# Optimization experiments

Hardware: AMD Instinct MI355X
Metric: run time of the kernel (lower is better)

## Reference

```python
import jax, jax.numpy as jnp
import numpy as np

B, D_IN, D, H, HD, M = 4096, 512, 128, 8, 16, 128
L = M + 1            # 1 query token + M memory slots
D_FF = 512
SCALE = 0.25         # 1/sqrt(HD)


def _ln(x, w, b, eps=1e-5):
    m = jnp.mean(x, axis=-1, keepdims=True)
    v = jnp.var(x, axis=-1, keepdims=True)
    return (x - m) * jax.lax.rsqrt(v + eps) * w + b


def setup_inputs() -> dict:
    ks = jax.random.split(jax.random.key(0), 26)
    n = lambda i, shape, s=1.0: jax.random.normal(ks[i], shape, jnp.float32) * s
    return {
        "x": n(0, (B, 1, D_IN)),
        "W_in": n(1, (D, D_IN), 0.05),
        "b_in": n(2, (D,), 0.02),
        "pos": n(3, (B, 1, D), 0.02),
        "mask": jnp.zeros((B, M), jnp.float32),  # additive attention bias for memory slots
        "mem": n(5, (B, M, D)),
        "ln1_w": jnp.ones((D,), jnp.float32), "ln1_b": jnp.zeros((D,), jnp.float32),
        "W_qkv": n(8, (3 * D, D), 0.09),
        "b_qkv": n(9, (3 * D,), 0.02),
        "W_out": n(10, (D, D), 0.09),
        "b_out": n(11, (D,), 0.02),
        "ln2_w": jnp.ones((D,), jnp.float32), "ln2_b": jnp.zeros((D,), jnp.float32),
        "ln3_w": jnp.ones((D,), jnp.float32), "ln3_b": jnp.zeros((D,), jnp.float32),
        "W_ff1": n(16, (D_FF, D), 0.09),
        "b_ff1": n(17, (D_FF,), 0.02),
        "ln4_w": jnp.ones((D_FF,), jnp.float32), "ln4_b": jnp.zeros((D_FF,), jnp.float32),
        "W_ff2": n(20, (D, D_FF), 0.04),
        "b_ff2": n(21, (D,), 0.02),
        "ln5_w": jnp.ones((D,), jnp.float32), "ln5_b": jnp.zeros((D,), jnp.float32),
        "W_head": n(24, (D_IN, D), 0.09),
        "b_head": n(25, (D_IN,), 0.02),
    }


def reference(x, W_in, b_in, pos, mask, mem, ln1_w, ln1_b, W_qkv, b_qkv,
              W_out, b_out, ln2_w, ln2_b, ln3_w, ln3_b, W_ff1, b_ff1,
              ln4_w, ln4_b, W_ff2, b_ff2, ln5_w, ln5_b, W_head, b_head):
    Bn = x.shape[0]
    # input projection + positional offset -> single query token per row  [B,1,D]
    q_in = (x.reshape(Bn, D_IN) @ W_in.T + b_in)[:, None, :] + pos
    # additive attention bias: 0 for the query slot, `mask` for memory slots  [B,L]
    bias = jnp.concatenate([jnp.zeros((Bn, 1), x.dtype), mask], axis=1)
    kv_in = jnp.concatenate([q_in, mem], axis=1)           # [B,L,D]
    kv_ln = _ln(kv_in, ln1_w, ln1_b)
    Wq, Wkv = W_qkv[:D], W_qkv[D:]
    bq, bkv = b_qkv[:D], b_qkv[D:]
    q = q_in[:, 0] @ Wq.T + bq                             # [B,D]  (Q uses UN-normalized q_in)
    kv = kv_ln @ Wkv.T + bkv                               # [B,L,2D]
    k, v = kv[..., :D], kv[..., D:]
    qh = q.reshape(Bn, H, HD)
    kh = k.reshape(Bn, L, H, HD)
    vh = v.reshape(Bn, L, H, HD)
    scores = jnp.einsum('bhd,blhd->bhl', qh * SCALE, kh) + bias[:, None, :]
    p = jax.nn.softmax(scores, axis=-1)                    # [B,H,L]
    o = jnp.einsum('bhl,blhd->bhd', p, vh).reshape(Bn, D)
    attn = _ln((o @ W_out.T + b_out)[:, None, :], ln2_w, ln2_b)
    h = attn + q_in                                        # residual  [B,1,D]
    f = _ln(h, ln3_w, ln3_b) @ W_ff1.T + b_ff1             # [B,1,D_FF]
    f = 0.5 * f * (1.0 + jax.lax.erf(f * 0.7071067811865476))  # exact GELU
    f = _ln(f, ln4_w, ln4_b) @ W_ff2.T + b_ff2             # [B,1,D]
    h2 = _ln(f + h, ln5_w, ln5_b)
    return h2 @ W_head.T + b_head                          # [B,1,D_IN]
```

## Files before the change

kernel.cpp:

```cpp
#include <hip/hip_runtime.h>

namespace {

constexpr int Dn   = 128;
constexpr int DIN  = 512;
constexpr int Hn   = 8;
constexpr int Mn   = 128;
constexpr int DFF  = 512;
constexpr int Gn   = 4;
constexpr float ATT_SCALE = 0.25f;
constexpr float INV_SQRT2 = 0.70710678118654752440f;

__device__ __forceinline__ float dot128(const float* __restrict__ wrow,
                                        const float* __restrict__ v)
{
    const float4* w4 = (const float4*)wrow;
    const float4* v4 = (const float4*)v;
    float acc = 0.f;
#pragma unroll
    for (int j = 0; j < 32; ++j) {
        float4 a = w4[j], b = v4[j];
        acc += a.x*b.x + a.y*b.y + a.z*b.z + a.w*b.w;
    }
    return acc;
}

template <int NCOL, int TPR>
__device__ __forceinline__ void ln_row(const float* __restrict__ src,
                                       float* __restrict__ dst,
                                       const float* __restrict__ gw,
                                       const float* __restrict__ gb,
                                       const float* __restrict__ resid,
                                       int sub)
{
    constexpr int E = NCOL / TPR;
    float v0[E]; float sm = 0.f;
#pragma unroll
    for (int i = 0; i < E; ++i) { v0[i] = src[sub*E + i]; sm += v0[i]; }
#pragma unroll
    for (int m = TPR/2; m >= 1; m >>= 1) sm += __shfl_xor(sm, m, TPR);
    float mean = sm * (1.f / (float)NCOL);
    float vs = 0.f;
#pragma unroll
    for (int i = 0; i < E; ++i) { float d0 = v0[i] - mean; vs += d0*d0; }
#pragma unroll
    for (int m = TPR/2; m >= 1; m >>= 1) vs += __shfl_xor(vs, m, TPR);
    float rstd = rsqrtf(vs * (1.f / (float)NCOL) + 1e-5f);
#pragma unroll
    for (int i = 0; i < E; ++i) {
        int d = sub*E + i;
        float r = (v0[i] - mean) * rstd * gw[d] + gb[d];
        dst[d] = resid ? (r + resid[d]) : r;
    }
}

__global__ __launch_bounds__(256, 2)
void fused_block(const float* __restrict__ x,
                 const float* __restrict__ W_in,
                 const float* __restrict__ b_in,
                 const float* __restrict__ pos,
                 const float* __restrict__ mask,
                 const float* __restrict__ mem,
                 const float* __restrict__ ln1_w, const float* __restrict__ ln1_b,
                 const float* __restrict__ W_qkv, const float* __restrict__ b_qkv,
                 const float* __restrict__ W_out, const float* __restrict__ b_out,
                 const float* __restrict__ ln2_w, const float* __restrict__ ln2_b,
                 const float* __restrict__ ln3_w, const float* __restrict__ ln3_b,
                 const float* __restrict__ W_ff1, const float* __restrict__ b_ff1,
                 const float* __restrict__ ln4_w, const float* __restrict__ ln4_b,
                 const float* __restrict__ W_ff2, const float* __restrict__ b_ff2,
                 const float* __restrict__ ln5_w, const float* __restrict__ ln5_b,
                 const float* __restrict__ W_head, const float* __restrict__ b_head,
                 float* __restrict__ out)
{
    const int t    = threadIdx.x;
    const int b0   = blockIdx.x * Gn;
    const int lane = t & 63;
    const int wv   = t >> 6;

    __shared__ __align__(16) float s_mem[Mn * Dn];
    __shared__ __align__(16) float s_A [Hn][Dn];
    __shared__ __align__(16) float s_sc[Hn][Mn];
    __shared__ __align__(16) float s_rstd[Mn];
    __shared__ __align__(16) float s_lnq[Dn];
    __shared__ __align__(16) float s_q  [Dn];
    __shared__ __align__(16) float s_qin[Gn][Dn];
    __shared__ __align__(16) float s_hh [Gn][Dn];
    __shared__ __align__(16) float s_qo [Gn][Dn];
    __shared__ float s_s1[Hn], s_s2c[Hn], s_s0[Hn], s_den[Hn], s_p0[Hn];

    float4* mem4 = (float4*)s_mem;
    float (*s_tmp)[Dn] = (float(*)[Dn])&s_sc[0][0];

    {
        const float4* src = (const float4*)(x + (size_t)b0 * DIN);
        mem4[t]       = src[t];
        mem4[t + 256] = src[t + 256];
    }
    __syncthreads();

    if (t < Dn) {
        const float4* w4 = (const float4*)(W_in + (size_t)t * DIN);
        float acc[Gn] = {0.f, 0.f, 0.f, 0.f};
        for (int j = 0; j < DIN/4; ++j) {
            float4 a = w4[j];
#pragma unroll
            for (int g = 0; g < Gn; ++g) {
                float4 xv = mem4[g*(DIN/4) + j];
                acc[g] = fmaf(a.x, xv.x, acc[g]); acc[g] = fmaf(a.y, xv.y, acc[g]);
                acc[g] = fmaf(a.z, xv.z, acc[g]); acc[g] = fmaf(a.w, xv.w, acc[g]);
            }
        }
#pragma unroll
        for (int g = 0; g < Gn; ++g)
            s_qin[g][t] = acc[g] + b_in[t] + pos[(size_t)(b0+g)*Dn + t];
    }
    __syncthreads();

    for (int g = 0; g < Gn; ++g) {
        __syncthreads();

        {
            const float4* src = (const float4*)(mem + (size_t)(b0+g) * Mn * Dn);
#pragma unroll
            for (int i = 0; i < 16; ++i) {
                int fid = t + 256*i;
                int r = fid >> 5, k = fid & 31;
                mem4[r*32 + (k ^ (r & 7))] = src[fid];
            }
        }
        if (t < 64) {
            ln_row<Dn, 64>(&s_qin[g][0], s_lnq, ln1_w, ln1_b, nullptr, t);
        } else if (t >= 128) {
            int dd = t - 128;
            s_q[dd] = dot128(W_qkv + (size_t)dd*Dn, &s_qin[g][0]) + b_qkv[dd];
        }
        __syncthreads();

        {
            int h = t >> 5, js = t & 31;
            float aq[4] = {0.f, 0.f, 0.f, 0.f};
            float ch = 0.f;
#pragma unroll
            for (int d0 = 0; d0 < 16; ++d0) {
                float qv = s_q[h*16 + d0];
                float4 w = ((const float4*)(W_qkv + (size_t)(Dn + h*16 + d0)*Dn))[js];
                aq[0] = fmaf(qv, w.x, aq[0]); aq[1] = fmaf(qv, w.y, aq[1]);
                aq[2] = fmaf(qv, w.z, aq[2]); aq[3] = fmaf(qv, w.w, aq[3]);
                ch = fmaf(qv, b_qkv[Dn + h*16 + d0], ch);
            }
            float s1p = 0.f, s2p = 0.f, s0p = 0.f;
            float aqw[4];
#pragma unroll
            for (int c = 0; c < 4; ++c) {
                int j = 4*js + c;
                float a = ATT_SCALE * aq[c];
                aqw[c] = a * ln1_w[j];
                s1p += aqw[c];
                s2p = fmaf(a, ln1_b[j], s2p);
                s0p = fmaf(a, s_lnq[j], s0p);
            }
            *(float4*)&s_A[h][4*js] = make_float4(aqw[0], aqw[1], aqw[2], aqw[3]);
            ch *= ATT_SCALE;
#pragma unroll
            for (int m = 16; m >= 1; m >>= 1) {
                s1p += __shfl_xor(s1p, m, 32);
                s2p += __shfl_xor(s2p, m, 32);
                s0p += __shfl_xor(s0p, m, 32);
            }
            if (js == 0) { s_s1[h] = s1p; s_s2c[h] = s2p + ch; s_s0[h] = s0p + ch; }
        }
        __syncthreads();
        {
            int h = t >> 5;
            float sub = s_s1[h] * (1.f/128.f);
            float4* p = (float4*)&s_A[0][0] + t;
            float4 v = *p;
            v.x -= sub; v.y -= sub; v.z -= sub; v.w -= sub;
            *p = v;
        }
        __syncthreads();

        {
            int r = t >> 1, hf = t & 1;
            float d[Hn];
#pragma unroll
            for (int h = 0; h < Hn; ++h) d[h] = 0.f;
            float sum = 0.f, ssq = 0.f;
#pragma unroll
            for (int kk = 0; kk < 16; ++kk) {
                int k = hf*16 + kk;
                float4 v = mem4[r*32 + (k ^ (r & 7))];
                sum += v.x + v.y + v.z + v.w;
                ssq = fmaf(v.x, v.x, ssq); ssq = fmaf(v.y, v.y, ssq);
                ssq = fmaf(v.z, v.z, ssq); ssq = fmaf(v.w, v.w, ssq);
#pragma unroll
                for (int h = 0; h < Hn; ++h) {
                    float4 a = ((const float4*)&s_A[h][0])[k];
                    d[h] = fmaf(a.x, v.x, d[h]); d[h] = fmaf(a.y, v.y, d[h]);
                    d[h] = fmaf(a.z, v.z, d[h]); d[h] = fmaf(a.w, v.w, d[h]);
                }
            }
            sum += __shfl_xor(sum, 1);
            ssq += __shfl_xor(ssq, 1);
#pragma unroll
            for (int h = 0; h < Hn; ++h) d[h] += __shfl_xor(d[h], 1);
            if (hf == 0) {
                float mean = sum * (1.f/128.f);
                float var  = fmaf(-mean, mean, ssq * (1.f/128.f));
                float rstd = rsqrtf(var + 1e-5f);
                float msk  = mask[(size_t)(b0+g)*Mn + r];
                s_rstd[r] = rstd;
#pragma unroll
                for (int h = 0; h < Hn; ++h)
                    s_sc[h][r] = fmaf(rstd, d[h], s_s2c[h]) + msk;
            }
        }
        __syncthreads();

        {
            int h = t >> 5, s = t & 31;
            float4 sv = ((float4*)&s_sc[h][0])[s];
            float s0 = s_s0[h];
            float mx = fmaxf(fmaxf(sv.x, sv.y), fmaxf(sv.z, sv.w));
#pragma unroll
            for (int m = 16; m >= 1; m >>= 1) mx = fmaxf(mx, __shfl_xor(mx, m, 32));
            mx = fmaxf(mx, s0);
            float e0 = __expf(sv.x - mx), e1 = __expf(sv.y - mx);
            float e2 = __expf(sv.z - mx), e3 = __expf(sv.w - mx);
            float ds = e0 + e1 + e2 + e3;
#pragma unroll
            for (int m = 16; m >= 1; m >>= 1) ds += __shfl_xor(ds, m, 32);
            float p0 = __expf(s0 - mx);
            float4 rs = ((float4*)s_rstd)[s];
            ((float4*)&s_sc[h][0])[s] =
                make_float4(e0*rs.x, e1*rs.y, e2*rs.z, e3*rs.w);
            if (s == 0) { s_den[h] = ds + p0; s_p0[h] = p0; }
        }
        __syncthreads();

        {
            int w = t >> 6, l = t & 63;
            int h0 = 2*w, h1 = 2*w + 1;
            int slot = l >> 1, half = l & 1;
            float c00 = 0.f, c01 = 0.f, c10 = 0.f, c11 = 0.f;
#pragma unroll 4
            for (int r = 0; r < Mn; ++r) {
                float2 mv = *(const float2*)(s_mem + r*Dn + ((slot ^ (r & 7)) << 2) + half*2);
                float q0 = s_sc[h0][r], q1 = s_sc[h1][r];
                c00 = fmaf(q0, mv.x, c00); c01 = fmaf(q0, mv.y, c01);
                c10 = fmaf(q1, mv.x, c10); c11 = fmaf(q1, mv.y, c11);
            }
            float r0 = c00 + c01, r1 = c10 + c11;
#pragma unroll
            for (int m = 1; m < 64; m <<= 1) {
                r0 += __shfl_xor(r0, m);
                r1 += __shfl_xor(r1, m);
            }
            float cS0 = r0 * (1.f/128.f), cS1 = r1 * (1.f/128.f);
            int j0 = 2*l, j1 = 2*l + 1;
            float den0 = s_den[h0], p00 = s_p0[h0], sP0 = den0 - p00, inv0 = 1.f/den0;
            float den1 = s_den[h1], p01 = s_p0[h1], sP1 = den1 - p01, inv1 = 1.f/den1;
            float lq0 = s_lnq[j0], lq1 = s_lnq[j1];
            float w0 = ln1_w[j0], w1 = ln1_w[j1];
            float bb0 = ln1_b[j0], bb1 = ln1_b[j1];
            *(float2*)&s_A[h0][j0] =
                make_float2((p00*lq0 + w0*(c00 - cS0) + bb0*sP0) * inv0,
                            (p00*lq1 + w1*(c01 - cS0) + bb1*sP0) * inv0);
            *(float2*)&s_A[h1][j0] =
                make_float2((p01*lq0 + w0*(c10 - cS1) + bb0*sP1) * inv1,
                            (p01*lq1 + w1*(c11 - cS1) + bb1*sP1) * inv1);
        }
        __syncthreads();

        if (t < Dn) {
            int h = t >> 4;
            s_qo[g][t] = dot128(W_qkv + (size_t)(2*Dn + t)*Dn, &s_A[h][0])
                       + b_qkv[2*Dn + t];
        }
    }
    __syncthreads();

    if (t < Dn) {
        const float4* w4 = (const float4*)(W_out + (size_t)t * Dn);
        float acc[Gn] = {0.f, 0.f, 0.f, 0.f};
#pragma unroll 8
        for (int j = 0; j < 32; ++j) {
            float4 a = w4[j];
#pragma unroll
            for (int g = 0; g < Gn; ++g) {
                float4 v = ((const float4*)&s_qo[g][0])[j];
                acc[g] = fmaf(a.x, v.x, acc[g]); acc[g] = fmaf(a.y, v.y, acc[g]);
                acc[g] = fmaf(a.z, v.z, acc[g]); acc[g] = fmaf(a.w, v.w, acc[g]);
            }
        }
#pragma unroll
        for (int g = 0; g < Gn; ++g) s_tmp[g][t] = acc[g] + b_out[t];
    }
    __syncthreads();

    ln_row<Dn, 64>(&s_tmp[wv][0], &s_hh[wv][0], ln2_w, ln2_b, &s_qin[wv][0], lane);
    __syncthreads();

    ln_row<Dn, 64>(&s_hh[wv][0], &s_qin[wv][0], ln3_w, ln3_b, nullptr, lane);
    __syncthreads();

    {
        int e0 = t, e1 = t + 256;
        const float4* wa = (const float4*)(W_ff1 + (size_t)e0 * Dn);
        const float4* wb = (const float4*)(W_ff1 + (size_t)e1 * Dn);
        float acc0[Gn] = {0.f,0.f,0.f,0.f}, acc1[Gn] = {0.f,0.f,0.f,0.f};
#pragma unroll 4
        for (int j = 0; j < 32; ++j) {
            float4 a = wa[j], b = wb[j];
#pragma unroll
            for (int g = 0; g < Gn; ++g) {
                float4 v = ((const float4*)&s_qin[g][0])[j];
                acc0[g] = fmaf(a.x, v.x, acc0[g]); acc0[g] = fmaf(a.y, v.y, acc0[g]);
                acc0[g] = fmaf(a.z, v.z, acc0[g]); acc0[g] = fmaf(a.w, v.w, acc0[g]);
                acc1[g] = fmaf(b.x, v.x, acc1[g]); acc1[g] = fmaf(b.y, v.y, acc1[g]);
                acc1[g] = fmaf(b.z, v.z, acc1[g]); acc1[g] = fmaf(b.w, v.w, acc1[g]);
            }
        }
#pragma unroll
        for (int g = 0; g < Gn; ++g) {
            float v0 = acc0[g] + b_ff1[e0];
            float v1 = acc1[g] + b_ff1[e1];
            s_mem[g*DFF + e0] = 0.5f * v0 * (1.f + erff(v0 * INV_SQRT2));
            s_mem[g*DFF + e1] = 0.5f * v1 * (1.f + erff(v1 * INV_SQRT2));
        }
    }
    __syncthreads();

    ln_row<DFF, 64>(s_mem + wv*DFF, s_mem + wv*DFF, ln4_w, ln4_b, nullptr, lane);
    __syncthreads();

    if (t < Dn) {
        const float4* w4 = (const float4*)(W_ff2 + (size_t)t * DFF);
        float acc[Gn] = {0.f, 0.f, 0.f, 0.f};
#pragma unroll 4
        for (int j = 0; j < DFF/4; ++j) {
            float4 a = w4[j];
#pragma unroll
            for (int g = 0; g < Gn; ++g) {
                float4 v = ((const float4*)(s_mem + g*DFF))[j];
                acc[g] = fmaf(a.x, v.x, acc[g]); acc[g] = fmaf(a.y, v.y, acc[g]);
                acc[g] = fmaf(a.z, v.z, acc[g]); acc[g] = fmaf(a.w, v.w, acc[g]);
            }
        }
#pragma unroll
        for (int g = 0; g < Gn; ++g)
            s_tmp[g][t] = acc[g] + b_ff2[t] + s_hh[g][t];
    }
    __syncthreads();

    ln_row<Dn, 64>(&s_tmp[wv][0], &s_qo[wv][0], ln5_w, ln5_b, nullptr, lane);
    __syncthreads();

    {
        int e0 = t, e1 = t + 256;
        const float4* wa = (const float4*)(W_head + (size_t)e0 * Dn);
        const float4* wb = (const float4*)(W_head + (size_t)e1 * Dn);
        float acc0[Gn] = {0.f,0.f,0.f,0.f}, acc1[Gn] = {0.f,0.f,0.f,0.f};
#pragma unroll 4
        for (int j = 0; j < 32; ++j) {
            float4 a = wa[j], b = wb[j];
#pragma unroll
            for (int g = 0; g < Gn; ++g) {
                float4 v = ((const float4*)&s_qo[g][0])[j];
                acc0[g] = fmaf(a.x, v.x, acc0[g]); acc0[g] = fmaf(a.y, v.y, acc0[g]);
                acc0[g] = fmaf(a.z, v.z, acc0[g]); acc0[g] = fmaf(a.w, v.w, acc0[g]);
                acc1[g] = fmaf(b.x, v.x, acc1[g]); acc1[g] = fmaf(b.y, v.y, acc1[g]);
                acc1[g] = fmaf(b.z, v.z, acc1[g]); acc1[g] = fmaf(b.w, v.w, acc1[g]);
            }
        }
#pragma unroll
        for (int g = 0; g < Gn; ++g) {
            out[(size_t)(b0+g)*DIN + e0] = acc0[g] + b_head[e0];
            out[(size_t)(b0+g)*DIN + e1] = acc1[g] + b_head[e1];
        }
    }
}

}

extern "C" void kernel_launch(void* const* d_in, const int* in_sizes, int n_in,
                              void* d_out, int out_size, void* d_ws, size_t ws_size,
                              hipStream_t stream)
{
    const float* x      = (const float*)d_in[0];
    const float* W_in   = (const float*)d_in[1];
    const float* b_in   = (const float*)d_in[2];
    const float* pos    = (const float*)d_in[3];
    const float* mask   = (const float*)d_in[4];
    const float* mem    = (const float*)d_in[5];
    const float* ln1_w  = (const float*)d_in[6];
    const float* ln1_b  = (const float*)d_in[7];
    const float* W_qkv  = (const float*)d_in[8];
    const float* b_qkv  = (const float*)d_in[9];
    const float* W_out  = (const float*)d_in[10];
    const float* b_out  = (const float*)d_in[11];
    const float* ln2_w  = (const float*)d_in[12];
    const float* ln2_b  = (const float*)d_in[13];
    const float* ln3_w  = (const float*)d_in[14];
    const float* ln3_b  = (const float*)d_in[15];
    const float* W_ff1  = (const float*)d_in[16];
    const float* b_ff1  = (const float*)d_in[17];
    const float* ln4_w  = (const float*)d_in[18];
    const float* ln4_b  = (const float*)d_in[19];
    const float* W_ff2  = (const float*)d_in[20];
    const float* b_ff2  = (const float*)d_in[21];
    const float* ln5_w  = (const float*)d_in[22];
    const float* ln5_b  = (const float*)d_in[23];
    const float* W_head = (const float*)d_in[24];
    const float* b_head = (const float*)d_in[25];

    const int B = in_sizes[0] / DIN;
    fused_block<<<dim3(B / Gn), dim3(256), 0, stream>>>(
        x, W_in, b_in, pos, mask, mem,
        ln1_w, ln1_b, W_qkv, b_qkv, W_out, b_out,
        ln2_w, ln2_b, ln3_w, ln3_b,
        W_ff1, b_ff1, ln4_w, ln4_b, W_ff2, b_ff2,
        ln5_w, ln5_b, W_head, b_head,
        (float*)d_out);
}
```

Baseline: 283.7 us.

## Process eight rows per block with 512 threads, split-K GEMVs and bf16 staging

Doubles the batch rows handled per block to eight and the block size to 512 threads, so each weight load is reused across more rows. The input and FF2 projections become split-K reductions through shared memory, the attention score and context stages are regrouped with one head per wave, and the per-head query-weight vector and attention output are stored in shared memory as bf16. This cuts global weight traffic per row and the number of barriers per row. In exchange it adds shared-memory reduction passes, precision loss from the bf16 rounding, and register pressure under the 512-thread launch bound.

```diff
diff --git a/kernel.cpp b/kernel.cpp
--- a/kernel.cpp
+++ b/kernel.cpp
@@ -7,9 +7,18 @@
 constexpr int Hn   = 8;
 constexpr int Mn   = 128;
 constexpr int DFF  = 512;
-constexpr int Gn   = 4;
+constexpr int Gn   = 8;
 constexpr float ATT_SCALE = 0.25f;
 constexpr float INV_SQRT2 = 0.70710678118654752440f;
+
+__device__ __forceinline__ unsigned short f2bf(float f) {
+    unsigned u = __float_as_uint(f);
+    unsigned r = (u + 0x7fffu + ((u >> 16) & 1u)) >> 16;
+    return (unsigned short)r;
+}
+__device__ __forceinline__ float bf2f(unsigned short s) {
+    return __uint_as_float((unsigned)s << 16);
+}
 
 __device__ __forceinline__ float dot128(const float* __restrict__ wrow,
                                         const float* __restrict__ v)
@@ -25,26 +34,26 @@
     return acc;
 }
 
-template <int NCOL, int TPR>
-__device__ __forceinline__ void ln_row(const float* __restrict__ src,
-                                       float* __restrict__ dst,
-                                       const float* __restrict__ gw,
-                                       const float* __restrict__ gb,
-                                       const float* __restrict__ resid,
-                                       int sub)
+template <int NCOL>
+__device__ __forceinline__ void ln_row64(const float* __restrict__ src,
+                                         float* __restrict__ dst,
+                                         const float* __restrict__ gw,
+                                         const float* __restrict__ gb,
+                                         const float* __restrict__ resid,
+                                         int sub)
 {
-    constexpr int E = NCOL / TPR;
+    constexpr int E = NCOL / 64;
     float v0[E]; float sm = 0.f;
 #pragma unroll
     for (int i = 0; i < E; ++i) { v0[i] = src[sub*E + i]; sm += v0[i]; }
 #pragma unroll
-    for (int m = TPR/2; m >= 1; m >>= 1) sm += __shfl_xor(sm, m, TPR);
+    for (int m = 32; m >= 1; m >>= 1) sm += __shfl_xor(sm, m);
     float mean = sm * (1.f / (float)NCOL);
     float vs = 0.f;
 #pragma unroll
     for (int i = 0; i < E; ++i) { float d0 = v0[i] - mean; vs += d0*d0; }
 #pragma unroll
-    for (int m = TPR/2; m >= 1; m >>= 1) vs += __shfl_xor(vs, m, TPR);
+    for (int m = 32; m >= 1; m >>= 1) vs += __shfl_xor(vs, m);
     float rstd = rsqrtf(vs * (1.f / (float)NCOL) + 1e-5f);
 #pragma unroll
     for (int i = 0; i < E; ++i) {
@@ -54,7 +63,7 @@
     }
 }
 
-__global__ __launch_bounds__(256, 2)
+__global__ __launch_bounds__(512, 2)
 void fused_block(const float* __restrict__ x,
                  const float* __restrict__ W_in,
                  const float* __restrict__ b_in,
@@ -79,67 +88,65 @@
     const int wv   = t >> 6;
 
     __shared__ __align__(16) float s_mem[Mn * Dn];
-    __shared__ __align__(16) float s_A [Hn][Dn];
-    __shared__ __align__(16) float s_sc[Hn][Mn];
-    __shared__ __align__(16) float s_rstd[Mn];
-    __shared__ __align__(16) float s_lnq[Dn];
-    __shared__ __align__(16) float s_q  [Dn];
+    __shared__ __align__(16) float s_A[1024];
+    __shared__ __align__(16) float s_sc[1152];
+    __shared__ __align__(16) float s_lnq[128];
     __shared__ __align__(16) float s_qin[Gn][Dn];
-    __shared__ __align__(16) float s_hh [Gn][Dn];
-    __shared__ __align__(16) float s_qo [Gn][Dn];
-    __shared__ float s_s1[Hn], s_s2c[Hn], s_s0[Hn], s_den[Hn], s_p0[Hn];
+    __shared__ __align__(16) unsigned short s_qo16[Gn][Dn];
+    __shared__ float s_s2c[Hn], s_s0[Hn], s_den[Hn], s_p0[Hn];
 
     float4* mem4 = (float4*)s_mem;
-    float (*s_tmp)[Dn] = (float(*)[Dn])&s_sc[0][0];
-
-    {
-        const float4* src = (const float4*)(x + (size_t)b0 * DIN);
-        mem4[t]       = src[t];
-        mem4[t + 256] = src[t + 256];
-    }
-    __syncthreads();
-
-    if (t < Dn) {
-        const float4* w4 = (const float4*)(W_in + (size_t)t * DIN);
-        float acc[Gn] = {0.f, 0.f, 0.f, 0.f};
-        for (int j = 0; j < DIN/4; ++j) {
+    unsigned short* s_At = (unsigned short*)s_A;
+    float* s_q = s_sc;
+
+    {
+        int d = t & 127, kg = t >> 7;
+        const float4* w4 = (const float4*)(W_in + (size_t)d * DIN) + kg*32;
+        float acc[8] = {0,0,0,0,0,0,0,0};
+        for (int j = 0; j < 32; ++j) {
             float4 a = w4[j];
 #pragma unroll
-            for (int g = 0; g < Gn; ++g) {
-                float4 xv = mem4[g*(DIN/4) + j];
+            for (int g = 0; g < 8; ++g) {
+                float4 xv = *(const float4*)(x + (size_t)(b0+g)*DIN + (size_t)(kg*32+j)*4);
                 acc[g] = fmaf(a.x, xv.x, acc[g]); acc[g] = fmaf(a.y, xv.y, acc[g]);
                 acc[g] = fmaf(a.z, xv.z, acc[g]); acc[g] = fmaf(a.w, xv.w, acc[g]);
             }
         }
 #pragma unroll
-        for (int g = 0; g < Gn; ++g)
-            s_qin[g][t] = acc[g] + b_in[t] + pos[(size_t)(b0+g)*Dn + t];
+        for (int g = 0; g < 8; ++g) s_mem[kg*1024 + d*8 + g] = acc[g];
+    }
+    __syncthreads();
+    {
+#pragma unroll
+        for (int u = 0; u < 2; ++u) {
+            int idx = t*2 + u; int d = idx >> 3, g = idx & 7;
+            float v = s_mem[idx] + s_mem[1024 + idx] + s_mem[2048 + idx] + s_mem[3072 + idx];
+            s_qin[g][d] = v + b_in[d] + pos[(size_t)(b0+g)*Dn + d];
+        }
     }
     __syncthreads();
 
     for (int g = 0; g < Gn; ++g) {
-        __syncthreads();
-
         {
             const float4* src = (const float4*)(mem + (size_t)(b0+g) * Mn * Dn);
 #pragma unroll
-            for (int i = 0; i < 16; ++i) {
-                int fid = t + 256*i;
+            for (int i = 0; i < 8; ++i) {
+                int fid = t + 512*i;
                 int r = fid >> 5, k = fid & 31;
                 mem4[r*32 + (k ^ (r & 7))] = src[fid];
             }
-        }
-        if (t < 64) {
-            ln_row<Dn, 64>(&s_qin[g][0], s_lnq, ln1_w, ln1_b, nullptr, t);
-        } else if (t >= 128) {
-            int dd = t - 128;
-            s_q[dd] = dot128(W_qkv + (size_t)dd*Dn, &s_qin[g][0]) + b_qkv[dd];
-        }
-        __syncthreads();
-
-        {
+            if (t < 64) {
+                ln_row64<Dn>(&s_qin[g][0], s_lnq, ln1_w, ln1_b, nullptr, t);
+            } else if (t >= 128 && t < 256) {
+                int dd = t - 128;
+                s_q[dd] = dot128(W_qkv + (size_t)dd*Dn, &s_qin[g][0]) + b_qkv[dd];
+            }
+        }
+        __syncthreads();
+
+        if (t < 256) {
             int h = t >> 5, js = t & 31;
-            float aq[4] = {0.f, 0.f, 0.f, 0.f};
+            float aq[4] = {0,0,0,0};
             float ch = 0.f;
 #pragma unroll
             for (int d0 = 0; d0 < 16; ++d0) {
@@ -149,235 +156,282 @@
                 aq[2] = fmaf(qv, w.z, aq[2]); aq[3] = fmaf(qv, w.w, aq[3]);
                 ch = fmaf(qv, b_qkv[Dn + h*16 + d0], ch);
             }
+            ch *= ATT_SCALE;
             float s1p = 0.f, s2p = 0.f, s0p = 0.f;
             float aqw[4];
 #pragma unroll
             for (int c = 0; c < 4; ++c) {
-                int j = 4*js + c;
+                int j = js*4 + c;
                 float a = ATT_SCALE * aq[c];
                 aqw[c] = a * ln1_w[j];
                 s1p += aqw[c];
                 s2p = fmaf(a, ln1_b[j], s2p);
                 s0p = fmaf(a, s_lnq[j], s0p);
             }
-            *(float4*)&s_A[h][4*js] = make_float4(aqw[0], aqw[1], aqw[2], aqw[3]);
-            ch *= ATT_SCALE;
 #pragma unroll
             for (int m = 16; m >= 1; m >>= 1) {
                 s1p += __shfl_xor(s1p, m, 32);
                 s2p += __shfl_xor(s2p, m, 32);
                 s0p += __shfl_xor(s0p, m, 32);
             }
-            if (js == 0) { s_s1[h] = s1p; s_s2c[h] = s2p + ch; s_s0[h] = s0p + ch; }
-        }
-        __syncthreads();
-        {
-            int h = t >> 5;
-            float sub = s_s1[h] * (1.f/128.f);
-            float4* p = (float4*)&s_A[0][0] + t;
-            float4 v = *p;
-            v.x -= sub; v.y -= sub; v.z -= sub; v.w -= sub;
-            *p = v;
-        }
-        __syncthreads();
-
-        {
-            int r = t >> 1, hf = t & 1;
-            float d[Hn];
-#pragma unroll
-            for (int h = 0; h < Hn; ++h) d[h] = 0.f;
+            float sub = s1p * (1.f/128.f);
+#pragma unroll
+            for (int c = 0; c < 4; ++c) {
+                int j = js*4 + c;
+                s_At[j*8 + h] = f2bf(aqw[c] - sub);
+            }
+            if (js == 0) { s_s2c[h] = s2p + ch; s_s0[h] = s0p + ch; }
+        }
+        __syncthreads();
+
+        {
+            int r = t >> 2, hf = t & 3;
+            float d8[8] = {0,0,0,0,0,0,0,0};
             float sum = 0.f, ssq = 0.f;
 #pragma unroll
-            for (int kk = 0; kk < 16; ++kk) {
-                int k = hf*16 + kk;
+            for (int kk = 0; kk < 8; ++kk) {
+                int k = hf*8 + kk;
                 float4 v = mem4[r*32 + (k ^ (r & 7))];
                 sum += v.x + v.y + v.z + v.w;
                 ssq = fmaf(v.x, v.x, ssq); ssq = fmaf(v.y, v.y, ssq);
                 ssq = fmaf(v.z, v.z, ssq); ssq = fmaf(v.w, v.w, ssq);
 #pragma unroll
-                for (int h = 0; h < Hn; ++h) {
-                    float4 a = ((const float4*)&s_A[h][0])[k];
-                    d[h] = fmaf(a.x, v.x, d[h]); d[h] = fmaf(a.y, v.y, d[h]);
-                    d[h] = fmaf(a.z, v.z, d[h]); d[h] = fmaf(a.w, v.w, d[h]);
+                for (int c = 0; c < 4; ++c) {
+                    int j = k*4 + c;
+                    uint4 au = *(const uint4*)&s_At[j*8];
+                    float a0 = __uint_as_float(au.x << 16);
+                    float a1 = __uint_as_float(au.x & 0xffff0000u);
+                    float a2 = __uint_as_float(au.y << 16);
+                    float a3 = __uint_as_float(au.y & 0xffff0000u);
+                    float a4 = __uint_as_float(au.z << 16);
+                    float a5 = __uint_as_float(au.z & 0xffff0000u);
+                    float a6 = __uint_as_float(au.w << 16);
+                    float a7 = __uint_as_float(au.w & 0xffff0000u);
+                    float vc = (c == 0) ? v.x : (c == 1) ? v.y : (c == 2) ? v.z : v.w;
+                    d8[0] = fmaf(a0, vc, d8[0]); d8[1] = fmaf(a1, vc, d8[1]);
+                    d8[2] = fmaf(a2, vc, d8[2]); d8[3] = fmaf(a3, vc, d8[3]);
+                    d8[4] = fmaf(a4, vc, d8[4]); d8[5] = fmaf(a5, vc, d8[5]);
+                    d8[6] = fmaf(a6, vc, d8[6]); d8[7] = fmaf(a7, vc, d8[7]);
                 }
             }
-            sum += __shfl_xor(sum, 1);
-            ssq += __shfl_xor(ssq, 1);
-#pragma unroll
-            for (int h = 0; h < Hn; ++h) d[h] += __shfl_xor(d[h], 1);
+#pragma unroll
+            for (int m = 1; m <= 2; m <<= 1) {
+                sum += __shfl_xor(sum, m, 4);
+                ssq += __shfl_xor(ssq, m, 4);
+#pragma unroll
+                for (int h = 0; h < 8; ++h) d8[h] += __shfl_xor(d8[h], m, 4);
+            }
             if (hf == 0) {
                 float mean = sum * (1.f/128.f);
                 float var  = fmaf(-mean, mean, ssq * (1.f/128.f));
                 float rstd = rsqrtf(var + 1e-5f);
-                float msk  = mask[(size_t)(b0+g)*Mn + r];
-                s_rstd[r] = rstd;
-#pragma unroll
-                for (int h = 0; h < Hn; ++h)
-                    s_sc[h][r] = fmaf(rstd, d[h], s_s2c[h]) + msk;
-            }
-        }
-        __syncthreads();
-
-        {
-            int h = t >> 5, s = t & 31;
-            float4 sv = ((float4*)&s_sc[h][0])[s];
-            float s0 = s_s0[h];
-            float mx = fmaxf(fmaxf(sv.x, sv.y), fmaxf(sv.z, sv.w));
-#pragma unroll
-            for (int m = 16; m >= 1; m >>= 1) mx = fmaxf(mx, __shfl_xor(mx, m, 32));
-            mx = fmaxf(mx, s0);
-            float e0 = __expf(sv.x - mx), e1 = __expf(sv.y - mx);
-            float e2 = __expf(sv.z - mx), e3 = __expf(sv.w - mx);
-            float ds = e0 + e1 + e2 + e3;
-#pragma unroll
-            for (int m = 16; m >= 1; m >>= 1) ds += __shfl_xor(ds, m, 32);
-            float p0 = __expf(s0 - mx);
-            float4 rs = ((float4*)s_rstd)[s];
-            ((float4*)&s_sc[h][0])[s] =
-                make_float4(e0*rs.x, e1*rs.y, e2*rs.z, e3*rs.w);
-            if (s == 0) { s_den[h] = ds + p0; s_p0[h] = p0; }
-        }
-        __syncthreads();
-
-        {
-            int w = t >> 6, l = t & 63;
-            int h0 = 2*w, h1 = 2*w + 1;
-            int slot = l >> 1, half = l & 1;
-            float c00 = 0.f, c01 = 0.f, c10 = 0.f, c11 = 0.f;
+#pragma unroll
+                for (int h = 0; h < 8; ++h) s_sc[r*9 + h] = d8[h];
+                s_sc[r*9 + 8] = rstd;
+            }
+        }
+        __syncthreads();
+
+        {
+            int w = wv, l = lane;
+            int r0 = 2*l, r1 = 2*l + 1;
+            float raw0 = s_sc[r0*9 + w], rs0 = s_sc[r0*9 + 8];
+            float raw1 = s_sc[r1*9 + w], rs1 = s_sc[r1*9 + 8];
+            float mk0 = mask[(size_t)(b0+g)*Mn + r0];
+            float mk1 = mask[(size_t)(b0+g)*Mn + r1];
+            float sc0 = fmaf(rs0, raw0, s_s2c[w]) + mk0;
+            float sc1 = fmaf(rs1, raw1, s_s2c[w]) + mk1;
+            float mx = fmaxf(sc0, sc1);
+#pragma unroll
+            for (int m = 1; m < 64; m <<= 1) mx = fmaxf(mx, __shfl_xor(mx, m));
+            mx = fmaxf(mx, s_s0[w]);
+            float e0 = __expf(sc0 - mx), e1 = __expf(sc1 - mx);
+            float ds = e0 + e1;
+#pragma unroll
+            for (int m = 1; m < 64; m <<= 1) ds += __shfl_xor(ds, m);
+            float p0 = __expf(s_s0[w] - mx);
+            s_A[r0*8 + w] = e0 * rs0;
+            s_A[r1*8 + w] = e1 * rs1;
+            if (l == 0) { s_den[w] = ds + p0; s_p0[w] = p0; }
+        }
+        __syncthreads();
+
+        float ctx0[8], ctx1[8];
+        {
+            int w = wv, l = lane;
+#pragma unroll
+            for (int h = 0; h < 8; ++h) { ctx0[h] = 0.f; ctx1[h] = 0.f; }
 #pragma unroll 4
-            for (int r = 0; r < Mn; ++r) {
-                float2 mv = *(const float2*)(s_mem + r*Dn + ((slot ^ (r & 7)) << 2) + half*2);
-                float q0 = s_sc[h0][r], q1 = s_sc[h1][r];
-                c00 = fmaf(q0, mv.x, c00); c01 = fmaf(q0, mv.y, c01);
-                c10 = fmaf(q1, mv.x, c10); c11 = fmaf(q1, mv.y, c11);
-            }
-            float r0 = c00 + c01, r1 = c10 + c11;
-#pragma unroll
-            for (int m = 1; m < 64; m <<= 1) {
-                r0 += __shfl_xor(r0, m);
-                r1 += __shfl_xor(r1, m);
-            }
-            float cS0 = r0 * (1.f/128.f), cS1 = r1 * (1.f/128.f);
-            int j0 = 2*l, j1 = 2*l + 1;
-            float den0 = s_den[h0], p00 = s_p0[h0], sP0 = den0 - p00, inv0 = 1.f/den0;
-            float den1 = s_den[h1], p01 = s_p0[h1], sP1 = den1 - p01, inv1 = 1.f/den1;
-            float lq0 = s_lnq[j0], lq1 = s_lnq[j1];
-            float w0 = ln1_w[j0], w1 = ln1_w[j1];
-            float bb0 = ln1_b[j0], bb1 = ln1_b[j1];
-            *(float2*)&s_A[h0][j0] =
-                make_float2((p00*lq0 + w0*(c00 - cS0) + bb0*sP0) * inv0,
-                            (p00*lq1 + w1*(c01 - cS0) + bb1*sP0) * inv0);
-            *(float2*)&s_A[h1][j0] =
-                make_float2((p01*lq0 + w0*(c10 - cS1) + bb0*sP1) * inv1,
-                            (p01*lq1 + w1*(c11 - cS1) + bb1*sP1) * inv1);
-        }
-        __syncthreads();
-
-        if (t < Dn) {
+            for (int rr = 0; rr < 16; ++rr) {
+                int r = w*16 + rr;
+                float4 qa = *(const float4*)&s_A[r*8];
+                float4 qb = *(const float4*)&s_A[r*8 + 4];
+                const float* bp = s_mem + r*Dn + (((l>>1) ^ (r & 7)) << 2) + (l & 1)*2;
+                float2 mv = *(const float2*)bp;
+                ctx0[0]=fmaf(qa.x,mv.x,ctx0[0]); ctx1[0]=fmaf(qa.x,mv.y,ctx1[0]);
+                ctx0[1]=fmaf(qa.y,mv.x,ctx0[1]); ctx1[1]=fmaf(qa.y,mv.y,ctx1[1]);
+                ctx0[2]=fmaf(qa.z,mv.x,ctx0[2]); ctx1[2]=fmaf(qa.z,mv.y,ctx1[2]);
+                ctx0[3]=fmaf(qa.w,mv.x,ctx0[3]); ctx1[3]=fmaf(qa.w,mv.y,ctx1[3]);
+                ctx0[4]=fmaf(qb.x,mv.x,ctx0[4]); ctx1[4]=fmaf(qb.x,mv.y,ctx1[4]);
+                ctx0[5]=fmaf(qb.y,mv.x,ctx0[5]); ctx1[5]=fmaf(qb.y,mv.y,ctx1[5]);
+                ctx0[6]=fmaf(qb.z,mv.x,ctx0[6]); ctx1[6]=fmaf(qb.z,mv.y,ctx1[6]);
+                ctx0[7]=fmaf(qb.w,mv.x,ctx0[7]); ctx1[7]=fmaf(qb.w,mv.y,ctx1[7]);
+            }
+        }
+        __syncthreads();
+        {
+            int w = wv, l = lane;
+            int lw = l ^ (w << 3);
+#pragma unroll
+            for (int h = 0; h < 8; ++h) {
+                s_mem[(h*2+0)*512 + w*64 + lw] = ctx0[h];
+                s_mem[(h*2+1)*512 + w*64 + lw] = ctx1[h];
+            }
+        }
+        __syncthreads();
+        {
+            int w = wv, l = lane;
+            float c0 = 0.f, c1 = 0.f;
+#pragma unroll
+            for (int w2 = 0; w2 < 8; ++w2) {
+                int lw = l ^ (w2 << 3);
+                c0 += s_mem[(w*2+0)*512 + w2*64 + lw];
+                c1 += s_mem[(w*2+1)*512 + w2*64 + lw];
+            }
+            float rsum = c0 + c1;
+#pragma unroll
+            for (int m = 1; m < 64; m <<= 1) rsum += __shfl_xor(rsum, m);
+            float cS  = rsum * (1.f/128.f);
+            float den = s_den[w], p0 = s_p0[w];
+            float sP  = den - p0, inv = 1.f / den;
+            int j0 = 2*l, j1 = j0 + 1;
+            float n0 = (p0*s_lnq[j0] + ln1_w[j0]*(c0 - cS) + ln1_b[j0]*sP) * inv;
+            float n1 = (p0*s_lnq[j1] + ln1_w[j1]*(c1 - cS) + ln1_b[j1]*sP) * inv;
+            s_sc[w*128 + j0] = n0;
+            s_sc[w*128 + j1] = n1;
+        }
+        __syncthreads();
+
+        if (t < 128) {
             int h = t >> 4;
-            s_qo[g][t] = dot128(W_qkv + (size_t)(2*Dn + t)*Dn, &s_A[h][0])
-                       + b_qkv[2*Dn + t];
-        }
-    }
-    __syncthreads();
-
-    if (t < Dn) {
-        const float4* w4 = (const float4*)(W_out + (size_t)t * Dn);
-        float acc[Gn] = {0.f, 0.f, 0.f, 0.f};
+            float o = dot128(W_qkv + (size_t)(2*Dn + t)*Dn, &s_sc[h*128]) + b_qkv[2*Dn + t];
+            s_qo16[g][t] = f2bf(o);
+        }
+        __syncthreads();
+    }
+
+    {
+        int d = t & 127, gp = t >> 7;
+        const float4* w4 = (const float4*)(W_out + (size_t)d * Dn);
+        float a0 = 0.f, a1 = 0.f;
 #pragma unroll 8
         for (int j = 0; j < 32; ++j) {
             float4 a = w4[j];
-#pragma unroll
-            for (int g = 0; g < Gn; ++g) {
-                float4 v = ((const float4*)&s_qo[g][0])[j];
-                acc[g] = fmaf(a.x, v.x, acc[g]); acc[g] = fmaf(a.y, v.y, acc[g]);
-                acc[g] = fmaf(a.z, v.z, acc[g]); acc[g] = fmaf(a.w, v.w, acc[g]);
-            }
-        }
-#pragma unroll
-        for (int g = 0; g < Gn; ++g) s_tmp[g][t] = acc[g] + b_out[t];
-    }
-    __syncthreads();
-
-    ln_row<Dn, 64>(&s_tmp[wv][0], &s_hh[wv][0], ln2_w, ln2_b, &s_qin[wv][0], lane);
-    __syncthreads();
-
-    ln_row<Dn, 64>(&s_hh[wv][0], &s_qin[wv][0], ln3_w, ln3_b, nullptr, lane);
-    __syncthreads();
-
-    {
-        int e0 = t, e1 = t + 256;
+            uint2 u0 = *(const uint2*)&s_qo16[gp*2][j*4];
+            uint2 u1 = *(const uint2*)&s_qo16[gp*2+1][j*4];
+            float o00 = __uint_as_float(u0.x << 16), o01 = __uint_as_float(u0.x & 0xffff0000u);
+            float o02 = __uint_as_float(u0.y << 16), o03 = __uint_as_float(u0.y & 0xffff0000u);
+            float o10 = __uint_as_float(u1.x << 16), o11 = __uint_as_float(u1.x & 0xffff0000u);
+            float o12 = __uint_as_float(u1.y << 16), o13 = __uint_as_float(u1.y & 0xffff0000u);
+            a0 = fmaf(a.x,o00,a0); a0 = fmaf(a.y,o01,a0); a0 = fmaf(a.z,o02,a0); a0 = fmaf(a.w,o03,a0);
+            a1 = fmaf(a.x,o10,a1); a1 = fmaf(a.y,o11,a1); a1 = fmaf(a.z,o12,a1); a1 = fmaf(a.w,o13,a1);
+        }
+        s_sc[(gp*2)*128 + d]   = a0 + b_out[d];
+        s_sc[(gp*2+1)*128 + d] = a1 + b_out[d];
+    }
+    __syncthreads();
+
+    ln_row64<Dn>(&s_sc[wv*128], &s_A[wv*128], ln2_w, ln2_b, &s_qin[wv][0], lane);
+    __syncthreads();
+    ln_row64<Dn>(&s_A[wv*128], &s_qin[wv][0], ln3_w, ln3_b, nullptr, lane);
+    __syncthreads();
+
+    {
+        int ep = t >> 1, gg = t & 1;
+        int e0 = 2*ep, e1 = e0 + 1;
         const float4* wa = (const float4*)(W_ff1 + (size_t)e0 * Dn);
         const float4* wb = (const float4*)(W_ff1 + (size_t)e1 * Dn);
-        float acc0[Gn] = {0.f,0.f,0.f,0.f}, acc1[Gn] = {0.f,0.f,0.f,0.f};
+        float acc0[4] = {0,0,0,0}, acc1[4] = {0,0,0,0};
 #pragma unroll 4
         for (int j = 0; j < 32; ++j) {
             float4 a = wa[j], b = wb[j];
 #pragma unroll
-            for (int g = 0; g < Gn; ++g) {
-                float4 v = ((const float4*)&s_qin[g][0])[j];
-                acc0[g] = fmaf(a.x, v.x, acc0[g]); acc0[g] = fmaf(a.y, v.y, acc0[g]);
-                acc0[g] = fmaf(a.z, v.z, acc0[g]); acc0[g] = fmaf(a.w, v.w, acc0[g]);
-                acc1[g] = fmaf(b.x, v.x, acc1[g]); acc1[g] = fmaf(b.y, v.y, acc1[g]);
-                acc1[g] = fmaf(b.z, v.z, acc1[g]); acc1[g] = fmaf(b.w, v.w, acc1[g]);
-            }
-        }
-#pragma unroll
-        for (int g = 0; g < Gn; ++g) {
-            float v0 = acc0[g] + b_ff1[e0];
-            float v1 = acc1[g] + b_ff1[e1];
-            s_mem[g*DFF + e0] = 0.5f * v0 * (1.f + erff(v0 * INV_SQRT2));
-            s_mem[g*DFF + e1] = 0.5f * v1 * (1.f + erff(v1 * INV_SQRT2));
-        }
-    }
-    __syncthreads();
-
-    ln_row<DFF, 64>(s_mem + wv*DFF, s_mem + wv*DFF, ln4_w, ln4_b, nullptr, lane);
-    __syncthreads();
-
-    if (t < Dn) {
-        const float4* w4 = (const float4*)(W_ff2 + (size_t)t * DFF);
-        float acc[Gn] = {0.f, 0.f, 0.f, 0.f};
-#pragma unroll 4
-        for (int j = 0; j < DFF/4; ++j) {
+            for (int q = 0; q < 4; ++q) {
+                float4 v = *(const float4*)&s_qin[gg*4 + q][j*4];
+                acc0[q] = fmaf(a.x,v.x,acc0[q]); acc0[q] = fmaf(a.y,v.y,acc0[q]);
+                acc0[q] = fmaf(a.z,v.z,acc0[q]); acc0[q] = fmaf(a.w,v.w,acc0[q]);
+                acc1[q] = fmaf(b.x,v.x,acc1[q]); acc1[q] = fmaf(b.y,v.y,acc1[q]);
+                acc1[q] = fmaf(b.z,v.z,acc1[q]); acc1[q] = fmaf(b.w,v.w,acc1[q]);
+            }
+        }
+#pragma unroll
+        for (int q = 0; q < 4; ++q) {
+            int gq = gg*4 + q;
+            float v0 = acc0[q] + b_ff1[e0];
+            float v1 = acc1[q] + b_ff1[e1];
+            v0 = 0.5f * v0 * (1.f + erff(v0 * INV_SQRT2));
+            v1 = 0.5f * v1 * (1.f + erff(v1 * INV_SQRT2));
+            *(float2*)&s_mem[gq*512 + e0] = make_float2(v0, v1);
+        }
+    }
+    __syncthreads();
+
+    ln_row64<DFF>(&s_mem[wv*512], &s_mem[wv*512], ln4_w, ln4_b, nullptr, lane);
+    __syncthreads();
+
+    {
+        int d = t & 127, kg = t >> 7;
+        const float4* w4 = (const float4*)(W_ff2 + (size_t)d * DFF) + kg*32;
+        float acc[8] = {0,0,0,0,0,0,0,0};
+        for (int j = 0; j < 32; ++j) {
             float4 a = w4[j];
 #pragma unroll
-            for (int g = 0; g < Gn; ++g) {
-                float4 v = ((const float4*)(s_mem + g*DFF))[j];
-                acc[g] = fmaf(a.x, v.x, acc[g]); acc[g] = fmaf(a.y, v.y, acc[g]);
-                acc[g] = fmaf(a.z, v.z, acc[g]); acc[g] = fmaf(a.w, v.w, acc[g]);
-            }
-        }
-#pragma unroll
-        for (int g = 0; g < Gn; ++g)
-            s_tmp[g][t] = acc[g] + b_ff2[t] + s_hh[g][t];
-    }
-    __syncthreads();
-
-    ln_row<Dn, 64>(&s_tmp[wv][0], &s_qo[wv][0], ln5_w, ln5_b, nullptr, lane);
-    __syncthreads();
-
-    {
-        int e0 = t, e1 = t + 256;
+            for (int g2 = 0; g2 < 8; ++g2) {
+                float4 v = *(const float4*)&s_mem[g2*512 + (kg*32+j)*4];
+                acc[g2] = fmaf(a.x,v.x,acc[g2]); acc[g2] = fmaf(a.y,v.y,acc[g2]);
+                acc[g2] = fmaf(a.z,v.z,acc[g2]); acc[g2] = fmaf(a.w,v.w,acc[g2]);
+            }
+        }
+#pragma unroll
+        for (int g2 = 0; g2 < 8; ++g2) s_mem[4096 + kg*1024 + d*8 + g2] = acc[g2];
+    }
+    __syncthreads();
+    {
+#pragma unroll
+        for (int u = 0; u < 2; ++u) {
+            int idx = t*2 + u; int d = idx >> 3, g2 = idx & 7;
+            float v = s_mem[4096 + idx] + s_mem[5120 + idx] + s_mem[6144 + idx] + s_mem[7168 + idx];
+            s_sc[g2*128 + d] = v + b_ff2[d] + s_A[g2*128 + d];
+        }
+    }
+    __syncthreads();
+
+    ln_row64<Dn>(&s_sc[wv*128], &s_qin[wv][0], ln5_w, ln5_b, nullptr, lane);
+    __syncthreads();
+
+    {
+        int ep = t >> 1, gg = t & 1;
+        int e0 = 2*ep, e1 = e0 + 1;
         const float4* wa = (const float4*)(W_head + (size_t)e0 * Dn);
         const float4* wb = (const float4*)(W_head + (size_t)e1 * Dn);
-        float acc0[Gn] = {0.f,0.f,0.f,0.f}, acc1[Gn] = {0.f,0.f,0.f,0.f};
+        float acc0[4] = {0,0,0,0}, acc1[4] = {0,0,0,0};
 #pragma unroll 4
         for (int j = 0; j < 32; ++j) {
             float4 a = wa[j], b = wb[j];
 #pragma unroll
-            for (int g = 0; g < Gn; ++g) {
-                float4 v = ((const float4*)&s_qo[g][0])[j];
-                acc0[g] = fmaf(a.x, v.x, acc0[g]); acc0[g] = fmaf(a.y, v.y, acc0[g]);
-                acc0[g] = fmaf(a.z, v.z, acc0[g]); acc0[g] = fmaf(a.w, v.w, acc0[g]);
-                acc1[g] = fmaf(b.x, v.x, acc1[g]); acc1[g] = fmaf(b.y, v.y, acc1[g]);
-                acc1[g] = fmaf(b.z, v.z, acc1[g]); acc1[g] = fmaf(b.w, v.w, acc1[g]);
-            }
-        }
-#pragma unroll
-        for (int g = 0; g < Gn; ++g) {
-            out[(size_t)(b0+g)*DIN + e0] = acc0[g] + b_head[e0];
-            out[(size_t)(b0+g)*DIN + e1] = acc1[g] + b_head[e1];
+            for (int q = 0; q < 4; ++q) {
+                float4 v = *(const float4*)&s_qin[gg*4 + q][j*4];
+                acc0[q] = fmaf(a.x,v.x,acc0[q]); acc0[q] = fmaf(a.y,v.y,acc0[q]);
+                acc0[q] = fmaf(a.z,v.z,acc0[q]); acc0[q] = fmaf(a.w,v.w,acc0[q]);
+                acc1[q] = fmaf(b.x,v.x,acc1[q]); acc1[q] = fmaf(b.y,v.y,acc1[q]);
+                acc1[q] = fmaf(b.z,v.z,acc1[q]); acc1[q] = fmaf(b.w,v.w,acc1[q]);
+            }
+        }
+#pragma unroll
+        for (int q = 0; q < 4; ++q) {
+            int gq = gg*4 + q;
+            *(float2*)&out[(size_t)(b0+gq)*DIN + e0] =
+                make_float2(acc0[q] + b_head[e0], acc1[q] + b_head[e1]);
         }
     }
 }
@@ -416,7 +470,7 @@
     const float* b_head = (const float*)d_in[25];
 
     const int B = in_sizes[0] / DIN;
-    fused_block<<<dim3(B / Gn), dim3(256), 0, stream>>>(
+    fused_block<<<dim3(B / Gn), dim3(512), 0, stream>>>(
         x, W_in, b_in, pos, mask, mem,
         ln1_w, ln1_b, W_qkv, b_qkv, W_out, b_out,
         ln2_w, ln2_b, ln3_w, ln3_b,
```

New measurement: 382.9 us. +35.0%, slower.
